# Kernel optimization log

Measured on AMD Instinct MI355X. Metric: run time of the kernel, lower is better.

## Reference

```python
import jax, jax.numpy as jnp
import numpy as np

D_MODEL = 1024
D_HEAD = 64
M_BITS = 32


def setup_inputs() -> dict:
    key = jax.random.key(0)
    ks = jax.random.split(key, 6)
    B, N, M = 2, 2048, 2048
    Q = jax.random.normal(ks[0], (B, N, D_MODEL), dtype=jnp.float32)
    K = jax.random.normal(ks[1], (B, M, D_MODEL), dtype=jnp.float32)
    V = jax.random.normal(ks[2], (B, M, D_MODEL), dtype=jnp.float32)
    s = 1.0 / np.sqrt(D_MODEL)
    Wq = jax.random.normal(ks[3], (D_MODEL, M_BITS), dtype=jnp.float32) * s
    Wk = jax.random.normal(ks[4], (D_MODEL, M_BITS), dtype=jnp.float32) * s
    Wv = jax.random.normal(ks[5], (D_MODEL, D_HEAD), dtype=jnp.float32) * s
    temperature = jnp.ones((1,), dtype=jnp.float32)
    return {"Q": Q, "K": K, "V": V, "Wq": Wq, "Wk": Wk, "Wv": Wv,
            "temperature": temperature}


def tropical_matmul(A, Bt):
    # A: [B, N, m], Bt: [B, M, m] (already transposed form of [B, m, M])
    # (A \odot B)_{ij} = min_k (A_ik + B_kj)
    return jnp.min(A[:, :, None, :] + Bt[:, None, :, :], axis=-1)  # [B, N, M]


def reference(Q, K, V, Wq, Wk, Wv, temperature):
    # REWA tropical encoders (continuous): linear projections to m_bits
    Qt = jnp.einsum('bnd,dm->bnm', Q, Wq)   # [B, N, m_bits]
    Kt = jnp.einsum('bsd,dm->bsm', K, Wk)   # [B, M, m_bits]
    Vp = jnp.einsum('bsd,dh->bsh', V, Wv)   # [B, M, d_head]
    # tropical (min-plus) scores, negated so shorter paths score higher
    scores = -tropical_matmul(Qt, Kt)       # [B, N, M]
    scores = scores / jax.nn.softplus(temperature[0])
    attn = jax.nn.softmax(scores, axis=-1)  # [B, N, M]
    out = jnp.einsum('bnm,bmh->bnh', attn, Vp)  # [B, N, d_head]
    return out, attn
```

## Files before the change

kernel.cpp:

```cpp
#include <hip/hip_runtime.h>
#include <math.h>

#define DM 1024
#define NB 2048
#define MBITS 32
#define DH 64

typedef __attribute__((ext_vector_type(4))) float floatx4;
typedef __attribute__((ext_vector_type(8))) short shortx8;

__device__ __forceinline__ unsigned short f32_to_bf16(float f) {
    union { float f; unsigned u; } v; v.f = f;
    unsigned r = v.u + 0x7FFF + ((v.u >> 16) & 1);
    return (unsigned short)(r >> 16);
}

__device__ __forceinline__ void split2(float x0, float x1, unsigned& hp, unsigned& lp) {
    union { float f; unsigned u; } a, b; a.f = x0; b.f = x1;
    unsigned h0 = a.u & 0xFFFF0000u, h1 = b.u & 0xFFFF0000u;
    union { unsigned u; float f; } hf0, hf1; hf0.u = h0; hf1.u = h1;
    union { float f; unsigned u; } c, d;
    c.f = x0 - hf0.f;
    d.f = x1 - hf1.f;
    hp = (h0 >> 16) | h1;
    lp = (c.u >> 16) | (d.u & 0xFFFF0000u);
}

__global__ __launch_bounds__(256) void wprep_kernel(
    const float* __restrict__ Wq, const float* __restrict__ Wk,
    const float* __restrict__ Wv, unsigned short* __restrict__ Wf)
{
    int wv = blockIdx.x * 4 + (threadIdx.x >> 6);
    int l  = threadIdx.x & 63;
    const float* W; int C, kc32, ct;
    if (wv < 64)       { W = Wq; C = 32; kc32 = wv >> 1;  ct = wv & 1; }
    else if (wv < 128) { W = Wk; C = 32; int z = wv - 64;  kc32 = z >> 1; ct = z & 1; }
    else               { W = Wv; C = 64; int z = wv - 128; kc32 = z >> 2; ct = z & 3; }
    int k0 = kc32 * 32 + (l >> 4) * 8;
    int c  = ct * 16 + (l & 15);
    float x[8];
    #pragma unroll
    for (int j = 0; j < 8; ++j) x[j] = W[(size_t)(k0 + j) * C + c];
    unsigned hp[4], lp[4];
    #pragma unroll
    for (int j2 = 0; j2 < 4; ++j2) split2(x[2 * j2], x[2 * j2 + 1], hp[j2], lp[j2]);
    uint4 hv; hv.x = hp[0]; hv.y = hp[1]; hv.z = hp[2]; hv.w = hp[3];
    uint4 lv; lv.x = lp[0]; lv.y = lp[1]; lv.z = lp[2]; lv.w = lp[3];
    *(uint4*)&Wf[(size_t)wv * 1024 + l * 8]       = hv;
    *(uint4*)&Wf[(size_t)wv * 1024 + 512 + l * 8] = lv;
}

__global__ __launch_bounds__(256) void proj_mfma2_kernel(
    const float* __restrict__ Q, const float* __restrict__ K, const float* __restrict__ V,
    const unsigned short* __restrict__ Wf,
    float* __restrict__ Qt, float* __restrict__ KtT, unsigned short* __restrict__ VpT)
{
    __shared__ float red[4][64][16];

    int gb = blockIdx.x;
    int job = gb >> 8, tile = gb & 255;
    int r0 = tile * 16;
    const float* X = (job == 0) ? Q : (job == 1) ? K : V;
    int ntct  = (job == 2) ? 4 : 2;
    int pbase = job << 6;
    int t = threadIdx.x, w = t >> 6, l = t & 63;
    int lrow = l & 15, lq = l >> 4;

    const float* xrow = &X[(size_t)(r0 + lrow) * DM + w * 256 + lq * 8];

    floatx4 acc[4];
    #pragma unroll
    for (int i = 0; i < 4; ++i) acc[i] = (floatx4){0.f, 0.f, 0.f, 0.f};

    #pragma unroll
    for (int s = 0; s < 8; ++s) {
        floatx4 g0 = *(const floatx4*)(xrow + s * 32);
        floatx4 g1 = *(const floatx4*)(xrow + s * 32 + 4);
        union { unsigned u[4]; shortx8 v; } ahi, alo;
        split2(g0.x, g0.y, ahi.u[0], alo.u[0]);
        split2(g0.z, g0.w, ahi.u[1], alo.u[1]);
        split2(g1.x, g1.y, ahi.u[2], alo.u[2]);
        split2(g1.z, g1.w, ahi.u[3], alo.u[3]);
        int kc32 = w * 8 + s;
        #pragma unroll
        for (int ct = 0; ct < 4; ++ct) {
            if (ct >= ntct) break;
            int p = pbase + kc32 * ntct + ct;
            const unsigned short* wp = &Wf[(size_t)p * 1024 + l * 8];
            shortx8 bhi = *(const shortx8*)wp;
            shortx8 blo = *(const shortx8*)(wp + 512);
            acc[ct] = __builtin_amdgcn_mfma_f32_16x16x32_bf16(ahi.v, bhi, acc[ct], 0, 0, 0);
            acc[ct] = __builtin_amdgcn_mfma_f32_16x16x32_bf16(ahi.v, blo, acc[ct], 0, 0, 0);
            acc[ct] = __builtin_amdgcn_mfma_f32_16x16x32_bf16(alo.v, bhi, acc[ct], 0, 0, 0);
        }
    }

    #pragma unroll
    for (int ct = 0; ct < 4; ++ct) {
        if (ct >= ntct) break;
        #pragma unroll
        for (int r = 0; r < 4; ++r) red[w][l][ct * 4 + r] = acc[ct][r];
    }
    __syncthreads();

    int row = r0 + lq * 4 + w;
    if (job == 0) {
        #pragma unroll
        for (int ct = 0; ct < 2; ++ct) {
            float v = red[0][l][ct * 4 + w] + red[1][l][ct * 4 + w]
                    + red[2][l][ct * 4 + w] + red[3][l][ct * 4 + w];
            Qt[(size_t)row * MBITS + ct * 16 + lrow] = v;
        }
    } else if (job == 1) {
        int bb = row >> 11, j = row & 2047;
        #pragma unroll
        for (int ct = 0; ct < 2; ++ct) {
            float v = red[0][l][ct * 4 + w] + red[1][l][ct * 4 + w]
                    + red[2][l][ct * 4 + w] + red[3][l][ct * 4 + w];
            KtT[(size_t)bb * (MBITS * NB) + (size_t)(ct * 16 + lrow) * NB + j] = v;
        }
    } else {
        int bb = row >> 11, j = row & 2047;
        #pragma unroll
        for (int ct = 0; ct < 4; ++ct) {
            float v = red[0][l][ct * 4 + w] + red[1][l][ct * 4 + w]
                    + red[2][l][ct * 4 + w] + red[3][l][ct * 4 + w];
            VpT[(size_t)bb * (DH * NB) + (size_t)(ct * 16 + lrow) * NB + j] = f32_to_bf16(v);
        }
    }
}

__global__ __attribute__((amdgpu_waves_per_eu(4, 4))) __launch_bounds__(1024)
void fused_score_out_kernel(
    const float* __restrict__ Qt, const float* __restrict__ KtT,
    const unsigned short* __restrict__ VpT, const float* __restrict__ temp,
    float* __restrict__ outp, float* __restrict__ attn)
{
    __shared__ unsigned short Elds[16][2056];
    __shared__ unsigned short Vsb[2][64][256];
    __shared__ float redsum2[16][2];
    __shared__ float inv_s[16];
    __shared__ float redC[16][64][4];

    const int b  = blockIdx.y;
    const int i0 = blockIdx.x * 16;
    const int t  = threadIdx.x;
    const int w  = t >> 6, l = t & 63;

    const float tv = temp[0];
    const float c2 = -(1.0f / log1pf(__expf(tv))) * 1.44269504088896340736f;

    {
        const int ip  = w & 7;
        const int jhb = (w >> 3) * 1024;
        const int p   = l >> 4;
        const int l16 = l & 15;

        const float* Qbase = &Qt[(size_t)(b * NB + i0 + ip * 2) * MBITS + p * 8];
        floatx4 qa0 = *(const floatx4*)(Qbase);
        floatx4 qa1 = *(const floatx4*)(Qbase + 4);
        floatx4 qb0 = *(const floatx4*)(Qbase + MBITS);
        floatx4 qb1 = *(const floatx4*)(Qbase + MBITS + 4);

        const float* Kp = &KtT[(size_t)b * (MBITS * NB) + (size_t)(p * 8) * NB];
        float sacc0 = 0.f, sacc1 = 0.f;

        #pragma unroll 1
        for (int s = 0; s < 8; ++s) {
            const int j0 = jhb + s * 128 + l16 * 8;
            float m0[8], m1[8];
            #pragma unroll
            for (int jj = 0; jj < 8; ++jj) { m0[jj] = 1e30f; m1[jj] = 1e30f; }

            #pragma unroll
            for (int kp = 0; kp < 8; ++kp) {
                const float* kr = Kp + (size_t)kp * NB + j0;
                floatx4 k0 = *(const floatx4*)kr;
                floatx4 k1 = *(const floatx4*)(kr + 4);
                float qa = (kp < 4) ? qa0[kp] : qa1[kp - 4];
                float qb = (kp < 4) ? qb0[kp] : qb1[kp - 4];
                float kv[8] = {k0.x, k0.y, k0.z, k0.w, k1.x, k1.y, k1.z, k1.w};
                #pragma unroll
                for (int jj = 0; jj < 8; ++jj) {
                    m0[jj] = fminf(m0[jj], qa + kv[jj]);
                    m1[jj] = fminf(m1[jj], qb + kv[jj]);
                }
            }
            #pragma unroll
            for (int jj = 0; jj < 8; ++jj) {
                m0[jj] = fminf(m0[jj], __shfl_xor(m0[jj], 16, 64));
                m0[jj] = fminf(m0[jj], __shfl_xor(m0[jj], 32, 64));
                m1[jj] = fminf(m1[jj], __shfl_xor(m1[jj], 16, 64));
                m1[jj] = fminf(m1[jj], __shfl_xor(m1[jj], 32, 64));
            }
            float e0[8], e1[8];
            #pragma unroll
            for (int jj = 0; jj < 8; ++jj) {
                e0[jj] = exp2f(c2 * m0[jj]);
                e1[jj] = exp2f(c2 * m1[jj]);
            }
            uint4 u0, u1;
            u0.x = (unsigned)f32_to_bf16(e0[0]) | ((unsigned)f32_to_bf16(e0[1]) << 16);
            u0.y = (unsigned)f32_to_bf16(e0[2]) | ((unsigned)f32_to_bf16(e0[3]) << 16);
            u0.z = (unsigned)f32_to_bf16(e0[4]) | ((unsigned)f32_to_bf16(e0[5]) << 16);
            u0.w = (unsigned)f32_to_bf16(e0[6]) | ((unsigned)f32_to_bf16(e0[7]) << 16);
            u1.x = (unsigned)f32_to_bf16(e1[0]) | ((unsigned)f32_to_bf16(e1[1]) << 16);
            u1.y = (unsigned)f32_to_bf16(e1[2]) | ((unsigned)f32_to_bf16(e1[3]) << 16);
            u1.z = (unsigned)f32_to_bf16(e1[4]) | ((unsigned)f32_to_bf16(e1[5]) << 16);
            u1.w = (unsigned)f32_to_bf16(e1[6]) | ((unsigned)f32_to_bf16(e1[7]) << 16);
            if (l < 16) {
                *(uint4*)&Elds[ip * 2][j0]     = u0;
                *(uint4*)&Elds[ip * 2 + 1][j0] = u1;
            }
            float s0 = ((e0[0] + e0[1]) + (e0[2] + e0[3])) + ((e0[4] + e0[5]) + (e0[6] + e0[7]));
            float s1 = ((e1[0] + e1[1]) + (e1[2] + e1[3])) + ((e1[4] + e1[5]) + (e1[6] + e1[7]));
            #pragma unroll
            for (int off = 1; off < 16; off <<= 1) {
                s0 += __shfl_xor(s0, off, 64);
                s1 += __shfl_xor(s1, off, 64);
            }
            sacc0 += s0; sacc1 += s1;
        }
        if (l == 0) { redsum2[w][0] = sacc0; redsum2[w][1] = sacc1; }
    }
    __syncthreads();

    if (t < 16) {
        inv_s[t] = 1.0f / (redsum2[t >> 1][t & 1] + redsum2[8 + (t >> 1)][t & 1]);
    }

    const int sh = t >> 5, sc = t & 31;
    {
        uint4 g0 = *(const uint4*)&VpT[(size_t)b * (DH * NB) + (size_t)sh * NB + sc * 8];
        uint4 g1 = *(const uint4*)&VpT[(size_t)b * (DH * NB) + (size_t)(sh + 32) * NB + sc * 8];
        *(uint4*)&Vsb[0][sh][(sc ^ (sh & 31)) * 8]             = g0;
        *(uint4*)&Vsb[0][sh + 32][(sc ^ ((sh + 32) & 31)) * 8] = g1;
    }
    __syncthreads();

    const int mrow = l & 15, q4 = l >> 4;
    const int hh  = (w & 3) * 16 + mrow;
    const int kg  = w >> 2;
    const int vsw = hh & 31;
    const float iv = inv_s[w];
    floatx4 acc = {0.f, 0.f, 0.f, 0.f};
    int pb = 0;

    for (int jc2 = 0; jc2 < 8; ++jc2) {
        uint4 g0, g1;
        if (jc2 < 7) {
            g0 = *(const uint4*)&VpT[(size_t)b * (DH * NB) + (size_t)sh * NB + (jc2 + 1) * 256 + sc * 8];
            g1 = *(const uint4*)&VpT[(size_t)b * (DH * NB) + (size_t)(sh + 32) * NB + (jc2 + 1) * 256 + sc * 8];
        }
        #pragma unroll
        for (int t2 = 0; t2 < 2; ++t2) {
            int ks = kg * 2 + t2;
            shortx8 a = *(const shortx8*)&Elds[mrow][jc2 * 256 + ks * 32 + q4 * 8];
            int c = ks * 4 + q4;
            shortx8 bf = *(const shortx8*)&Vsb[pb][hh][(c ^ vsw) * 8];
            acc = __builtin_amdgcn_mfma_f32_16x16x32_bf16(a, bf, acc, 0, 0, 0);
        }
        {
            uint2 pk = *(const uint2*)&Elds[w][jc2 * 256 + l * 4];
            union { unsigned u; float f; } x0, x1, x2, x3;
            x0.u = pk.x << 16; x1.u = pk.x & 0xFFFF0000u;
            x2.u = pk.y << 16; x3.u = pk.y & 0xFFFF0000u;
            floatx4 o;
            o.x = x0.f * iv; o.y = x1.f * iv; o.z = x2.f * iv; o.w = x3.f * iv;
            *(floatx4*)&attn[(size_t)(b * NB + i0 + w) * 2048 + jc2 * 256 + l * 4] = o;
        }
        if (jc2 < 7) {
            *(uint4*)&Vsb[pb ^ 1][sh][(sc ^ (sh & 31)) * 8]             = g0;
            *(uint4*)&Vsb[pb ^ 1][sh + 32][(sc ^ ((sh + 32) & 31)) * 8] = g1;
        }
        __syncthreads();
        pb ^= 1;
    }

    *(floatx4*)&redC[w][l][0] = acc;
    __syncthreads();
    if (w < 4) {
        floatx4 v0 = *(const floatx4*)&redC[w][l][0];
        floatx4 v1 = *(const floatx4*)&redC[w + 4][l][0];
        floatx4 v2 = *(const floatx4*)&redC[w + 8][l][0];
        floatx4 v3 = *(const floatx4*)&redC[w + 12][l][0];
        #pragma unroll
        for (int r = 0; r < 4; ++r) {
            int irow = q4 * 4 + r;
            float v = (v0[r] + v1[r]) + (v2[r] + v3[r]);
            outp[(size_t)(b * NB + i0 + irow) * DH + w * 16 + mrow] = v * inv_s[irow];
        }
    }
}

extern "C" void kernel_launch(void* const* d_in, const int* in_sizes, int n_in,
                              void* d_out, int out_size, void* d_ws, size_t ws_size,
                              hipStream_t stream) {
    (void)in_sizes; (void)n_in; (void)out_size; (void)ws_size;
    const float* Q    = (const float*)d_in[0];
    const float* K    = (const float*)d_in[1];
    const float* V    = (const float*)d_in[2];
    const float* Wq   = (const float*)d_in[3];
    const float* Wk   = (const float*)d_in[4];
    const float* Wv   = (const float*)d_in[5];
    const float* temp = (const float*)d_in[6];

    float* outp = (float*)d_out;
    float* attn = outp + 2 * 2048 * 64;

    char* ws = (char*)d_ws;
    float*          Qt  = (float*)(ws);
    float*          KtT = (float*)(ws + 524288);
    unsigned short* Wf  = (unsigned short*)(ws + 1179648);
    unsigned short* VpT = (unsigned short*)(ws + 1703936);

    wprep_kernel<<<64, 256, 0, stream>>>(Wq, Wk, Wv, Wf);
    proj_mfma2_kernel<<<768, 256, 0, stream>>>(Q, K, V, Wf, Qt, KtT, VpT);
    fused_score_out_kernel<<<dim3(128, 2), 1024, 0, stream>>>(Qt, KtT, VpT, temp, outp, attn);
}
```

Baseline: 151.4 us.

## Halve query rows per block, read V directly from global, drop LDS staging

The fused score/output kernel now handles 8 query rows per block instead of 16 and launches twice as many blocks. The 16 waves are split four ways over the key dimension rather than two. The double-buffered LDS staging of V is replaced by direct global loads of the B operand, which removes the per-chunk barriers. The unused rows of the MFMA A tile are zero-filled, so half the MFMA work is spent on padding. The attn write-out and the row normalisation are regrouped to fit the new layout, and the waves_per_eu hint is removed.

```diff
diff --git a/kernel.cpp b/kernel.cpp
--- a/kernel.cpp
+++ b/kernel.cpp
@@ -130,29 +130,32 @@
     }
 }
 
-__global__ __attribute__((amdgpu_waves_per_eu(4, 4))) __launch_bounds__(1024)
-void fused_score_out_kernel(
+__global__ __launch_bounds__(1024) void fused_score_out_kernel(
     const float* __restrict__ Qt, const float* __restrict__ KtT,
     const unsigned short* __restrict__ VpT, const float* __restrict__ temp,
     float* __restrict__ outp, float* __restrict__ attn)
 {
     __shared__ unsigned short Elds[16][2056];
-    __shared__ unsigned short Vsb[2][64][256];
     __shared__ float redsum2[16][2];
-    __shared__ float inv_s[16];
-    __shared__ float redC[16][64][4];
+    __shared__ float redC[12][64][4];
 
     const int b  = blockIdx.y;
-    const int i0 = blockIdx.x * 16;
+    const int i0 = blockIdx.x * 8;
     const int t  = threadIdx.x;
     const int w  = t >> 6, l = t & 63;
 
+    {
+        uint4 z; z.x = 0; z.y = 0; z.z = 0; z.w = 0;
+        uint4* base = (uint4*)&Elds[8][0];
+        for (int zi = t; zi < 2056; zi += 1024) base[zi] = z;
+    }
+
     const float tv = temp[0];
     const float c2 = -(1.0f / log1pf(__expf(tv))) * 1.44269504088896340736f;
 
     {
-        const int ip  = w & 7;
-        const int jhb = (w >> 3) * 1024;
+        const int ip  = w & 3;
+        const int jqb = (w >> 2) * 512;
         const int p   = l >> 4;
         const int l16 = l & 15;
 
@@ -166,8 +169,8 @@
         float sacc0 = 0.f, sacc1 = 0.f;
 
         #pragma unroll 1
-        for (int s = 0; s < 8; ++s) {
-            const int j0 = jhb + s * 128 + l16 * 8;
+        for (int s = 0; s < 4; ++s) {
+            const int j0 = jqb + s * 128 + l16 * 8;
             float m0[8], m1[8];
             #pragma unroll
             for (int jj = 0; jj < 8; ++jj) { m0[jj] = 1e30f; m1[jj] = 1e30f; }
@@ -225,70 +228,57 @@
     }
     __syncthreads();
 
-    if (t < 16) {
-        inv_s[t] = 1.0f / (redsum2[t >> 1][t & 1] + redsum2[8 + (t >> 1)][t & 1]);
-    }
-
-    const int sh = t >> 5, sc = t & 31;
-    {
-        uint4 g0 = *(const uint4*)&VpT[(size_t)b * (DH * NB) + (size_t)sh * NB + sc * 8];
-        uint4 g1 = *(const uint4*)&VpT[(size_t)b * (DH * NB) + (size_t)(sh + 32) * NB + sc * 8];
-        *(uint4*)&Vsb[0][sh][(sc ^ (sh & 31)) * 8]             = g0;
-        *(uint4*)&Vsb[0][sh + 32][(sc ^ ((sh + 32) & 31)) * 8] = g1;
-    }
-    __syncthreads();
-
     const int mrow = l & 15, q4 = l >> 4;
     const int hh  = (w & 3) * 16 + mrow;
     const int kg  = w >> 2;
-    const int vsw = hh & 31;
-    const float iv = inv_s[w];
     floatx4 acc = {0.f, 0.f, 0.f, 0.f};
-    int pb = 0;
-
+    const unsigned short* Vb = &VpT[(size_t)b * (DH * NB) + (size_t)hh * NB];
+
+    #pragma unroll
     for (int jc2 = 0; jc2 < 8; ++jc2) {
-        uint4 g0, g1;
-        if (jc2 < 7) {
-            g0 = *(const uint4*)&VpT[(size_t)b * (DH * NB) + (size_t)sh * NB + (jc2 + 1) * 256 + sc * 8];
-            g1 = *(const uint4*)&VpT[(size_t)b * (DH * NB) + (size_t)(sh + 32) * NB + (jc2 + 1) * 256 + sc * 8];
-        }
         #pragma unroll
         for (int t2 = 0; t2 < 2; ++t2) {
             int ks = kg * 2 + t2;
-            shortx8 a = *(const shortx8*)&Elds[mrow][jc2 * 256 + ks * 32 + q4 * 8];
-            int c = ks * 4 + q4;
-            shortx8 bf = *(const shortx8*)&Vsb[pb][hh][(c ^ vsw) * 8];
+            int joff = jc2 * 256 + ks * 32 + q4 * 8;
+            shortx8 a  = *(const shortx8*)&Elds[mrow][joff];
+            shortx8 bf = *(const shortx8*)&Vb[joff];
             acc = __builtin_amdgcn_mfma_f32_16x16x32_bf16(a, bf, acc, 0, 0, 0);
         }
-        {
-            uint2 pk = *(const uint2*)&Elds[w][jc2 * 256 + l * 4];
+    }
+
+    {
+        const int rw = w & 7, jh = w >> 3, rp = rw >> 1, rq = rw & 1;
+        float iv = 1.0f / ((redsum2[rp][rq] + redsum2[4 + rp][rq])
+                         + (redsum2[8 + rp][rq] + redsum2[12 + rp][rq]));
+        #pragma unroll
+        for (int u = 0; u < 4; ++u) {
+            int j = jh * 1024 + u * 256 + l * 4;
+            uint2 pk = *(const uint2*)&Elds[rw][j];
             union { unsigned u; float f; } x0, x1, x2, x3;
             x0.u = pk.x << 16; x1.u = pk.x & 0xFFFF0000u;
             x2.u = pk.y << 16; x3.u = pk.y & 0xFFFF0000u;
             floatx4 o;
             o.x = x0.f * iv; o.y = x1.f * iv; o.z = x2.f * iv; o.w = x3.f * iv;
-            *(floatx4*)&attn[(size_t)(b * NB + i0 + w) * 2048 + jc2 * 256 + l * 4] = o;
-        }
-        if (jc2 < 7) {
-            *(uint4*)&Vsb[pb ^ 1][sh][(sc ^ (sh & 31)) * 8]             = g0;
-            *(uint4*)&Vsb[pb ^ 1][sh + 32][(sc ^ ((sh + 32) & 31)) * 8] = g1;
-        }
-        __syncthreads();
-        pb ^= 1;
-    }
-
-    *(floatx4*)&redC[w][l][0] = acc;
+            *(floatx4*)&attn[(size_t)(b * NB + i0 + rw) * 2048 + j] = o;
+        }
+    }
+
+    if (w >= 4) *(floatx4*)&redC[w - 4][l][0] = acc;
     __syncthreads();
     if (w < 4) {
         floatx4 v0 = *(const floatx4*)&redC[w][l][0];
         floatx4 v1 = *(const floatx4*)&redC[w + 4][l][0];
         floatx4 v2 = *(const floatx4*)&redC[w + 8][l][0];
-        floatx4 v3 = *(const floatx4*)&redC[w + 12][l][0];
-        #pragma unroll
-        for (int r = 0; r < 4; ++r) {
-            int irow = q4 * 4 + r;
-            float v = (v0[r] + v1[r]) + (v2[r] + v3[r]);
-            outp[(size_t)(b * NB + i0 + irow) * DH + w * 16 + mrow] = v * inv_s[irow];
+        if (l < 32) {
+            #pragma unroll
+            for (int r = 0; r < 4; ++r) {
+                int irow = q4 * 4 + r;
+                int rp = irow >> 1, rq = irow & 1;
+                float ivr = 1.0f / ((redsum2[rp][rq] + redsum2[4 + rp][rq])
+                                  + (redsum2[8 + rp][rq] + redsum2[12 + rp][rq]));
+                float v = ((acc[r] + v0[r]) + (v1[r] + v2[r]));
+                outp[(size_t)(b * NB + i0 + irow) * DH + w * 16 + mrow] = v * ivr;
+            }
         }
     }
 }
@@ -316,5 +306,5 @@
 
     wprep_kernel<<<64, 256, 0, stream>>>(Wq, Wk, Wv, Wf);
     proj_mfma2_kernel<<<768, 256, 0, stream>>>(Q, K, V, Wf, Qt, KtT, VpT);
-    fused_score_out_kernel<<<dim3(128, 2), 1024, 0, stream>>>(Qt, KtT, VpT, temp, outp, attn);
-}
+    fused_score_out_kernel<<<dim3(256, 2), 1024, 0, stream>>>(Qt, KtT, VpT, temp, outp, attn);
+}
```

Result: slower. 161.7 us (+6.8%).
